# Optimization experiments

Hardware: AMD Instinct MI355X
Metric: run time of the kernel (lower is better)

Reference implementation:

```python
import jax, jax.numpy as jnp
import numpy as np

KH, KW = 3, 3
PAD = (1, 1, 1, 1)  # torch F.pad order: (W_left, W_right, H_top, H_bottom)
STRIDE = 1
B, CIN, COUT, H, W = 4, 32, 32, 128, 128


def setup_inputs() -> dict:
    key = jax.random.key(0)
    k1, k2, k3, k4 = jax.random.split(key, 4)
    f = jax.random.normal(k1, (B, CIN, H, W), jnp.float32)
    # orientation field components (cos/sin of a random angle field)
    theta = jax.random.uniform(k2, (B, CIN, H, W), jnp.float32, 0.0, 2.0 * np.pi)
    r0 = jnp.cos(theta)
    r1 = jnp.sin(theta)
    # learned conv weight (nn.Conv2d default uniform init, no bias)
    fan_in = CIN * KH * KW
    bound = 1.0 / np.sqrt(fan_in)
    w = jax.random.uniform(k3, (COUT, CIN, KH, KW), jnp.float32, -bound, bound)
    # frozen wr: (randn * pi * 100) / a with a = 100  ->  randn * pi
    wr = jax.random.normal(k4, (COUT, CIN, KH, KW), jnp.float32) * np.pi
    return {"f": f, "r0": r0, "r1": r1, "w": w, "wr": wr}


def _rot90(w):
    # torch: w.permute(0,1,2,4,3).flip([4]) on the (kh,kw) dims
    return jnp.flip(jnp.swapaxes(w, -1, -2), -1)


def _conv_single(f, r0, r1, w, wr):
    # f, r0, r1: (B, Cin, Hp, Wp);  w, wr: (Cout, Cin, KH, KW)
    Hp, Wp = f.shape[2], f.shape[3]
    he = Hp - PAD[0] - PAD[1]
    we = Wp - PAD[2] - PAD[3]
    s = STRIDE
    out = None
    for i in range(KH):
        for j in range(KW):
            fw = f[:, :, i:i + he:s, j:j + we:s]    # (B, Cin, h, w)
            r0w = r0[:, :, i:i + he:s, j:j + we:s]
            r1w = r1[:, :, i:i + he:s, j:j + we:s]
            c = jnp.cos(wr[:, :, i, j])[None, :, :, None, None]   # (1, Cout, Cin, 1, 1)
            sn = jnp.sin(wr[:, :, i, j])[None, :, :, None, None]
            # lambda_theta: relu of orientation-projected field, (B, Cout, Cin, h, w)
            lam = jax.nn.relu(c * r0w[:, None] + sn * r1w[:, None])
            term = jnp.einsum('bchw,oc,bochw->bohw', fw, w[:, :, i, j], lam)
            out = term if out is None else out + term
    return out  # (B, Cout, h, w)


def _forward(f, r0, r1, w, wr):
    pl, pr, pt, pb = PAD
    pad = ((0, 0), (0, 0), (pt, pb), (pl, pr))
    fp = jnp.pad(f, pad)
    r0p = jnp.pad(r0, pad)
    r1p = jnp.pad(r1, pad)
    orient = jnp.arange(4, dtype=f.dtype) * jnp.asarray(np.pi / 2, f.dtype)
    outs = []
    wk = w
    for o in range(4):
        if o > 0:
            wk = _rot90(wk)
        outs.append(_conv_single(fp, r0p, r1p, wk, wr + orient[o]))
    stacked = jnp.stack(outs, axis=2)              # (B, Cout, 4, h, w)
    idx = jnp.argmax(stacked, axis=2)              # (B, Cout, h, w)
    out = jnp.take_along_axis(stacked, idx[:, :, None], axis=2)[:, :, 0]
    out_r = orient[idx]                            # winning orientation angle
    return out, jnp.cos(out_r), jnp.sin(out_r)


def reference(f, r0, r1, w, wr):
    return _forward(f, r0, r1, w, wr)
```

## Files before the change

### kernel.cpp

```cpp
#include <hip/hip_runtime.h>


typedef float v2f __attribute__((ext_vector_type(2)));

#define B_    4
#define CIN_  32
#define COUT_ 32
#define H_    128
#define W_    128
#define HW_   (H_ * W_)
#define OUTSZ_ (B_ * COUT_ * H_ * W_)

__global__ __launch_bounds__(256)
void build_wtab(const float* __restrict__ w, const float* __restrict__ wr,
                float* __restrict__ tab)
{
    int idx = blockIdx.x * 256 + threadIdx.x;
    if (idx >= CIN_ * 9 * COUT_) return;
    int oc  = idx & 31;
    int t2  = idx >> 5;
    int tap = t2 % 9;
    int cc  = t2 / 9;
    int i = tap / 3, j = tap - i * 3;
    int base = (oc * CIN_ + cc) * 9;
    float w0 = w[base + i * 3 + j];
    float w1 = w[base + (2 - j) * 3 + i];
    float w2 = w[base + (2 - i) * 3 + (2 - j)];
    float w3 = w[base + j * 3 + (2 - i)];
    float S, C;
    sincosf(wr[base + i * 3 + j], &S, &C);
    float* dst = tab + (size_t)idx * 8;
    dst[0] = C;  dst[1] = S;
    dst[2] = w0; dst[3] = w1;
    dst[4] = w2; dst[5] = w3;
    dst[6] = 0.0f; dst[7] = 0.0f;
}

#define NC_    8
#define NG_    (CIN_ / NC_)
#define ROWF_  68
#define CLSTR_ (3 * ROWF_)
#define USED_  (NC_ * CLSTR_)
#define PLANE_ 1636
#define BUF_   (3 * PLANE_)

__global__ __launch_bounds__(512, 4)
void orient_conv_kernel(const float* __restrict__ f,
                        const float* __restrict__ r0,
                        const float* __restrict__ r1,
                        const float* __restrict__ tab,
                        float* __restrict__ out)
{
    __shared__ float sm[2 * BUF_];

    const int tid   = threadIdx.x;
    const int oc    = tid & 31;
    const int pxg   = tid >> 5;
    const int p     = pxg << 1;
    const int bid   = blockIdx.x;
    const int b     = bid >> 8;
    const int rem   = bid & 255;
    const int h     = rem >> 1;
    const int wbase = (rem & 1) << 6;

    int      goff[4], sidx[4];
    unsigned msk[4];
#pragma unroll
    for (int k = 0; k < 4; ++k) {
        int s = tid + (k << 9);
        if (s < USED_) {
            int cl  = s / CLSTR_;
            int r2  = s - cl * CLSTR_;
            int row = r2 / ROWF_;
            int q2  = r2 - row * ROWF_;
            int col = (q2 >> 1) + ((q2 & 1) << 5);
            int gh = h + row - 1;
            int gw = wbase + col - 1;
            bool ok = ((unsigned)gh < (unsigned)H_) & ((unsigned)gw < (unsigned)W_);
            goff[k] = ok ? (cl * HW_ + gh * W_ + gw) : 0;
            msk[k]  = ok ? 0xFFFFFFFFu : 0u;
            sidx[k] = s;
        } else { goff[k] = 0; msk[k] = 0u; sidx[k] = USED_; }
    }
    const bool have3 = (tid + 1536) < USED_;
    const int chanBase = b * (CIN_ * HW_);

    v2f acc[2][4];
#pragma unroll
    for (int q = 0; q < 2; ++q)
#pragma unroll
        for (int o = 0; o < 4; ++o) acc[q][o] = (v2f)(0.0f);

    float tF[4], tA[4], tB[4];
    {
        const float* fb = f  + chanBase;
        const float* ab = r0 + chanBase;
        const float* bb = r1 + chanBase;
#pragma unroll
        for (int k = 0; k < 3; ++k) {
            tF[k] = fb[goff[k]]; tA[k] = ab[goff[k]]; tB[k] = bb[goff[k]];
        }
        if (have3) { tF[3] = fb[goff[3]]; tA[3] = ab[goff[3]]; tB[3] = bb[goff[3]]; }
    }
    {
        float* bw = sm;
#pragma unroll
        for (int k = 0; k < 3; ++k) {
            bw[             sidx[k]] = __uint_as_float(__float_as_uint(tF[k]) & msk[k]);
            bw[PLANE_     + sidx[k]] = __uint_as_float(__float_as_uint(tA[k]) & msk[k]);
            bw[2 * PLANE_ + sidx[k]] = __uint_as_float(__float_as_uint(tB[k]) & msk[k]);
        }
        if (have3) {
            bw[             sidx[3]] = __uint_as_float(__float_as_uint(tF[3]) & msk[3]);
            bw[PLANE_     + sidx[3]] = __uint_as_float(__float_as_uint(tA[3]) & msk[3]);
            bw[2 * PLANE_ + sidx[3]] = __uint_as_float(__float_as_uint(tB[3]) & msk[3]);
        }
    }
    __syncthreads();

#pragma unroll 1
    for (int g = 0; g < NG_; ++g) {
        if (g + 1 < NG_) {
            const int gb = chanBase + (g + 1) * (NC_ * HW_);
            const float* fb = f  + gb;
            const float* ab = r0 + gb;
            const float* bb = r1 + gb;
#pragma unroll
            for (int k = 0; k < 3; ++k) {
                tF[k] = fb[goff[k]]; tA[k] = ab[goff[k]]; tB[k] = bb[goff[k]];
            }
            if (have3) { tF[3] = fb[goff[3]]; tA[3] = ab[goff[3]]; tB[3] = bb[goff[3]]; }
        }

        const float* br = sm + (g & 1) * BUF_;
#pragma unroll 1
        for (int cl = 0; cl < NC_; ++cl) {
            const int cc = g * NC_ + cl;
            const float* wb0 = tab + (size_t)(((cc * 9 + 2) << 5) | oc) * 8;
            const float* wb1 = wb0 + 4 * 256;
#pragma unroll
            for (int i = 0; i < 3; ++i) {
                const int bi = cl * CLSTR_ + i * ROWF_ + (p << 1);
                float4 fA = *reinterpret_cast<const float4*>(&br[bi]);
                float4 fB = *reinterpret_cast<const float4*>(&br[bi + 4]);
                float4 aA = *reinterpret_cast<const float4*>(&br[PLANE_ + bi]);
                float4 aB = *reinterpret_cast<const float4*>(&br[PLANE_ + bi + 4]);
                float4 bA = *reinterpret_cast<const float4*>(&br[2 * PLANE_ + bi]);
                float4 bB = *reinterpret_cast<const float4*>(&br[2 * PLANE_ + bi + 4]);
                v2f fP[4]  = {{fA.x, fA.y}, {fA.z, fA.w}, {fB.x, fB.y}, {fB.z, fB.w}};
                v2f aP[4]  = {{aA.x, aA.y}, {aA.z, aA.w}, {aB.x, aB.y}, {aB.z, aB.w}};
                v2f bP[4]  = {{bA.x, bA.y}, {bA.z, bA.w}, {bB.x, bB.y}, {bB.z, bB.w}};
#pragma unroll
                for (int j = 0; j < 3; ++j) {
                    const int tap = i * 3 + j;
                    const float* wp = (tap < 5) ? (wb0 + (tap - 2) * 256)
                                                : (wb1 + (tap - 6) * 256);
                    float4 W4 = *reinterpret_cast<const float4*>(wp);
                    float2 W2 = *reinterpret_cast<const float2*>(wp + 4);
                    v2f C2  = {W4.x, W4.x};
                    v2f S2  = {W4.y, W4.y};
                    v2f w02 = {W4.z, W4.z};
                    v2f w12 = {W4.w, W4.w};
                    v2f w22 = {W2.x, W2.x};
                    v2f w32 = {W2.y, W2.y};
#pragma unroll
                    for (int q = 0; q < 2; ++q) {
                        v2f fv  = fP[q + j];
                        v2f r0v = aP[q + j];
                        v2f r1v = bP[q + j];
                        v2f m1 = S2 * r1v;
                        v2f u  = __builtin_elementwise_fma(C2, r0v, m1);
                        v2f m2 = S2 * r0v;
                        v2f vv = __builtin_elementwise_fma(C2, r1v, -m2);
                        v2f g0 = __builtin_elementwise_max(u,  (v2f)(0.0f));
                        v2f g1 = __builtin_elementwise_max(vv, (v2f)(0.0f));
                        v2f t0 = fv * g0;
                        v2f t1 = fv * g1;
                        v2f t2 = __builtin_elementwise_fma(fv, -u,  t0);
                        v2f t3 = __builtin_elementwise_fma(fv, -vv, t1);
                        acc[q][0] = __builtin_elementwise_fma(t0, w02, acc[q][0]);
                        acc[q][1] = __builtin_elementwise_fma(t1, w12, acc[q][1]);
                        acc[q][2] = __builtin_elementwise_fma(t2, w22, acc[q][2]);
                        acc[q][3] = __builtin_elementwise_fma(t3, w32, acc[q][3]);
                    }
                }
            }
        }

        if (g + 1 < NG_) {
            float* bw = sm + ((g + 1) & 1) * BUF_;
#pragma unroll
            for (int k = 0; k < 3; ++k) {
                bw[             sidx[k]] = __uint_as_float(__float_as_uint(tF[k]) & msk[k]);
                bw[PLANE_     + sidx[k]] = __uint_as_float(__float_as_uint(tA[k]) & msk[k]);
                bw[2 * PLANE_ + sidx[k]] = __uint_as_float(__float_as_uint(tB[k]) & msk[k]);
            }
            if (have3) {
                bw[             sidx[3]] = __uint_as_float(__float_as_uint(tF[3]) & msk[3]);
                bw[PLANE_     + sidx[3]] = __uint_as_float(__float_as_uint(tA[3]) & msk[3]);
                bw[2 * PLANE_ + sidx[3]] = __uint_as_float(__float_as_uint(tB[3]) & msk[3]);
            }
            __syncthreads();
        }
    }

    const float cosv[4] = {1.0f, -4.37113883e-08f, -1.0f, 1.19248806e-08f};
    const float sinv[4] = {0.0f, 1.0f, -8.74227766e-08f, -1.0f};
#pragma unroll
    for (int q = 0; q < 2; ++q) {
#pragma unroll
        for (int k = 0; k < 2; ++k) {
            int wcol = wbase + p + q + (k << 5);
            float a0 = acc[q][0][k], a1 = acc[q][1][k];
            float a2 = acc[q][2][k], a3 = acc[q][3][k];
            float best = a0; int bi = 0;
            if (a1 > best) { best = a1; bi = 1; }
            if (a2 > best) { best = a2; bi = 2; }
            if (a3 > best) { best = a3; bi = 3; }
            size_t o = ((size_t)(b * COUT_ + oc) * H_ + h) * W_ + wcol;
            out[o]              = best;
            out[o + OUTSZ_]     = cosv[bi];
            out[o + 2 * OUTSZ_] = sinv[bi];
        }
    }
}

extern "C" void kernel_launch(void* const* d_in, const int* in_sizes, int n_in,
                              void* d_out, int out_size, void* d_ws, size_t ws_size,
                              hipStream_t stream)
{
    const float* f  = (const float*)d_in[0];
    const float* r0 = (const float*)d_in[1];
    const float* r1 = (const float*)d_in[2];
    const float* w  = (const float*)d_in[3];
    const float* wr = (const float*)d_in[4];
    float* out = (float*)d_out;
    float* tab = (float*)d_ws;

    build_wtab<<<dim3(36), dim3(256), 0, stream>>>(w, wr, tab);
    orient_conv_kernel<<<dim3(B_ * H_ * 2), dim3(512), 0, stream>>>(
        f, r0, r1, tab, out);
}
```

Measured before the change: 288.9 us.

## Compute two output rows per block to reuse staged input rows

Each block now loads a 4-row halo per channel instead of 3 and produces two output rows, so each shared-memory row read feeds both output rows' taps. This cuts redundant global and LDS input traffic per output by about a third and halves the block count. In exchange it doubles the accumulator registers, drops the min-blocks launch bound hint, and enlarges shared memory per block, which may reduce occupancy and leave fewer blocks to fill the GPU.

Result: slower. 507.4 us (+75.6%).

```diff
diff --git a/kernel.cpp b/kernel.cpp
--- a/kernel.cpp
+++ b/kernel.cpp
@@ -39,12 +39,14 @@
 #define NC_    8
 #define NG_    (CIN_ / NC_)
 #define ROWF_  68
-#define CLSTR_ (3 * ROWF_)
+#define NROW_  4
+#define CLSTR_ (NROW_ * ROWF_)
 #define USED_  (NC_ * CLSTR_)
-#define PLANE_ 1636
+#define PLANE_ 2180
 #define BUF_   (3 * PLANE_)
-
-__global__ __launch_bounds__(512, 4)
+#define NRND_  5
+
+__global__ __launch_bounds__(512)
 void orient_conv_kernel(const float* __restrict__ f,
                         const float* __restrict__ r0,
                         const float* __restrict__ r1,
@@ -58,15 +60,15 @@
     const int pxg   = tid >> 5;
     const int p     = pxg << 1;
     const int bid   = blockIdx.x;
-    const int b     = bid >> 8;
-    const int rem   = bid & 255;
-    const int h     = rem >> 1;
+    const int b     = bid >> 7;
+    const int rem   = bid & 127;
+    const int h0    = (rem >> 1) << 1;
     const int wbase = (rem & 1) << 6;
 
-    int      goff[4], sidx[4];
-    unsigned msk[4];
-#pragma unroll
-    for (int k = 0; k < 4; ++k) {
+    int      goff[NRND_], sidx[NRND_];
+    unsigned msk[NRND_];
+#pragma unroll
+    for (int k = 0; k < NRND_; ++k) {
         int s = tid + (k << 9);
         if (s < USED_) {
             int cl  = s / CLSTR_;
@@ -74,7 +76,7 @@
             int row = r2 / ROWF_;
             int q2  = r2 - row * ROWF_;
             int col = (q2 >> 1) + ((q2 & 1) << 5);
-            int gh = h + row - 1;
+            int gh = h0 + row - 1;
             int gw = wbase + col - 1;
             bool ok = ((unsigned)gh < (unsigned)H_) & ((unsigned)gw < (unsigned)W_);
             goff[k] = ok ? (cl * HW_ + gh * W_ + gw) : 0;
@@ -82,38 +84,42 @@
             sidx[k] = s;
         } else { goff[k] = 0; msk[k] = 0u; sidx[k] = USED_; }
     }
-    const bool have3 = (tid + 1536) < USED_;
+    const bool have4 = (tid + 2048) < USED_;
     const int chanBase = b * (CIN_ * HW_);
 
-    v2f acc[2][4];
-#pragma unroll
-    for (int q = 0; q < 2; ++q)
-#pragma unroll
-        for (int o = 0; o < 4; ++o) acc[q][o] = (v2f)(0.0f);
-
-    float tF[4], tA[4], tB[4];
+    v2f acc[2][2][4];
+#pragma unroll
+    for (int rr = 0; rr < 2; ++rr)
+#pragma unroll
+        for (int q = 0; q < 2; ++q)
+#pragma unroll
+            for (int o = 0; o < 4; ++o) acc[rr][q][o] = (v2f)(0.0f);
+
+    float tF[NRND_], tA[NRND_], tB[NRND_];
     {
         const float* fb = f  + chanBase;
         const float* ab = r0 + chanBase;
         const float* bb = r1 + chanBase;
 #pragma unroll
-        for (int k = 0; k < 3; ++k) {
+        for (int k = 0; k < NRND_ - 1; ++k) {
             tF[k] = fb[goff[k]]; tA[k] = ab[goff[k]]; tB[k] = bb[goff[k]];
         }
-        if (have3) { tF[3] = fb[goff[3]]; tA[3] = ab[goff[3]]; tB[3] = bb[goff[3]]; }
+        if (have4) {
+            tF[4] = fb[goff[4]]; tA[4] = ab[goff[4]]; tB[4] = bb[goff[4]];
+        }
     }
     {
         float* bw = sm;
 #pragma unroll
-        for (int k = 0; k < 3; ++k) {
+        for (int k = 0; k < NRND_ - 1; ++k) {
             bw[             sidx[k]] = __uint_as_float(__float_as_uint(tF[k]) & msk[k]);
             bw[PLANE_     + sidx[k]] = __uint_as_float(__float_as_uint(tA[k]) & msk[k]);
             bw[2 * PLANE_ + sidx[k]] = __uint_as_float(__float_as_uint(tB[k]) & msk[k]);
         }
-        if (have3) {
-            bw[             sidx[3]] = __uint_as_float(__float_as_uint(tF[3]) & msk[3]);
-            bw[PLANE_     + sidx[3]] = __uint_as_float(__float_as_uint(tA[3]) & msk[3]);
-            bw[2 * PLANE_ + sidx[3]] = __uint_as_float(__float_as_uint(tB[3]) & msk[3]);
+        if (have4) {
+            bw[             sidx[4]] = __uint_as_float(__float_as_uint(tF[4]) & msk[4]);
+            bw[PLANE_     + sidx[4]] = __uint_as_float(__float_as_uint(tA[4]) & msk[4]);
+            bw[2 * PLANE_ + sidx[4]] = __uint_as_float(__float_as_uint(tB[4]) & msk[4]);
         }
     }
     __syncthreads();
@@ -126,10 +132,12 @@
             const float* ab = r0 + gb;
             const float* bb = r1 + gb;
 #pragma unroll
-            for (int k = 0; k < 3; ++k) {
+            for (int k = 0; k < NRND_ - 1; ++k) {
                 tF[k] = fb[goff[k]]; tA[k] = ab[goff[k]]; tB[k] = bb[goff[k]];
             }
-            if (have3) { tF[3] = fb[goff[3]]; tA[3] = ab[goff[3]]; tB[3] = bb[goff[3]]; }
+            if (have4) {
+                tF[4] = fb[goff[4]]; tA[4] = ab[goff[4]]; tB[4] = bb[goff[4]];
+            }
         }
 
         const float* br = sm + (g & 1) * BUF_;
@@ -139,8 +147,8 @@
             const float* wb0 = tab + (size_t)(((cc * 9 + 2) << 5) | oc) * 8;
             const float* wb1 = wb0 + 4 * 256;
 #pragma unroll
-            for (int i = 0; i < 3; ++i) {
-                const int bi = cl * CLSTR_ + i * ROWF_ + (p << 1);
+            for (int r = 0; r < NROW_; ++r) {
+                const int bi = cl * CLSTR_ + r * ROWF_ + (p << 1);
                 float4 fA = *reinterpret_cast<const float4*>(&br[bi]);
                 float4 fB = *reinterpret_cast<const float4*>(&br[bi + 4]);
                 float4 aA = *reinterpret_cast<const float4*>(&br[PLANE_ + bi]);
@@ -150,55 +158,60 @@
                 v2f fP[4]  = {{fA.x, fA.y}, {fA.z, fA.w}, {fB.x, fB.y}, {fB.z, fB.w}};
                 v2f aP[4]  = {{aA.x, aA.y}, {aA.z, aA.w}, {aB.x, aB.y}, {aB.z, aB.w}};
                 v2f bP[4]  = {{bA.x, bA.y}, {bA.z, bA.w}, {bB.x, bB.y}, {bB.z, bB.w}};
-#pragma unroll
-                for (int j = 0; j < 3; ++j) {
-                    const int tap = i * 3 + j;
-                    const float* wp = (tap < 5) ? (wb0 + (tap - 2) * 256)
-                                                : (wb1 + (tap - 6) * 256);
-                    float4 W4 = *reinterpret_cast<const float4*>(wp);
-                    float2 W2 = *reinterpret_cast<const float2*>(wp + 4);
-                    v2f C2  = {W4.x, W4.x};
-                    v2f S2  = {W4.y, W4.y};
-                    v2f w02 = {W4.z, W4.z};
-                    v2f w12 = {W4.w, W4.w};
-                    v2f w22 = {W2.x, W2.x};
-                    v2f w32 = {W2.y, W2.y};
-#pragma unroll
-                    for (int q = 0; q < 2; ++q) {
-                        v2f fv  = fP[q + j];
-                        v2f r0v = aP[q + j];
-                        v2f r1v = bP[q + j];
-                        v2f m1 = S2 * r1v;
-                        v2f u  = __builtin_elementwise_fma(C2, r0v, m1);
-                        v2f m2 = S2 * r0v;
-                        v2f vv = __builtin_elementwise_fma(C2, r1v, -m2);
-                        v2f g0 = __builtin_elementwise_max(u,  (v2f)(0.0f));
-                        v2f g1 = __builtin_elementwise_max(vv, (v2f)(0.0f));
-                        v2f t0 = fv * g0;
-                        v2f t1 = fv * g1;
-                        v2f t2 = __builtin_elementwise_fma(fv, -u,  t0);
-                        v2f t3 = __builtin_elementwise_fma(fv, -vv, t1);
-                        acc[q][0] = __builtin_elementwise_fma(t0, w02, acc[q][0]);
-                        acc[q][1] = __builtin_elementwise_fma(t1, w12, acc[q][1]);
-                        acc[q][2] = __builtin_elementwise_fma(t2, w22, acc[q][2]);
-                        acc[q][3] = __builtin_elementwise_fma(t3, w32, acc[q][3]);
+
+                auto apply = [&](int ti, int rr) {
+#pragma unroll
+                    for (int j = 0; j < 3; ++j) {
+                        const int tap = ti * 3 + j;
+                        const float* wp = (tap < 5) ? (wb0 + (tap - 2) * 256)
+                                                    : (wb1 + (tap - 6) * 256);
+                        float4 W4 = *reinterpret_cast<const float4*>(wp);
+                        float2 W2 = *reinterpret_cast<const float2*>(wp + 4);
+                        v2f C2  = {W4.x, W4.x};
+                        v2f S2  = {W4.y, W4.y};
+                        v2f w02 = {W4.z, W4.z};
+                        v2f w12 = {W4.w, W4.w};
+                        v2f w22 = {W2.x, W2.x};
+                        v2f w32 = {W2.y, W2.y};
+#pragma unroll
+                        for (int q = 0; q < 2; ++q) {
+                            v2f fv  = fP[q + j];
+                            v2f r0v = aP[q + j];
+                            v2f r1v = bP[q + j];
+                            v2f m1 = S2 * r1v;
+                            v2f u  = __builtin_elementwise_fma(C2, r0v, m1);
+                            v2f m2 = S2 * r0v;
+                            v2f vv = __builtin_elementwise_fma(C2, r1v, -m2);
+                            v2f g0 = __builtin_elementwise_max(u,  (v2f)(0.0f));
+                            v2f g1 = __builtin_elementwise_max(vv, (v2f)(0.0f));
+                            v2f t0 = fv * g0;
+                            v2f t1 = fv * g1;
+                            v2f t2 = __builtin_elementwise_fma(fv, -u,  t0);
+                            v2f t3 = __builtin_elementwise_fma(fv, -vv, t1);
+                            acc[rr][q][0] = __builtin_elementwise_fma(t0, w02, acc[rr][q][0]);
+                            acc[rr][q][1] = __builtin_elementwise_fma(t1, w12, acc[rr][q][1]);
+                            acc[rr][q][2] = __builtin_elementwise_fma(t2, w22, acc[rr][q][2]);
+                            acc[rr][q][3] = __builtin_elementwise_fma(t3, w32, acc[rr][q][3]);
+                        }
                     }
-                }
+                };
+                if (r < 3) apply(r, 0);
+                if (r > 0) apply(r - 1, 1);
             }
         }
 
         if (g + 1 < NG_) {
             float* bw = sm + ((g + 1) & 1) * BUF_;
 #pragma unroll
-            for (int k = 0; k < 3; ++k) {
+            for (int k = 0; k < NRND_ - 1; ++k) {
                 bw[             sidx[k]] = __uint_as_float(__float_as_uint(tF[k]) & msk[k]);
                 bw[PLANE_     + sidx[k]] = __uint_as_float(__float_as_uint(tA[k]) & msk[k]);
                 bw[2 * PLANE_ + sidx[k]] = __uint_as_float(__float_as_uint(tB[k]) & msk[k]);
             }
-            if (have3) {
-                bw[             sidx[3]] = __uint_as_float(__float_as_uint(tF[3]) & msk[3]);
-                bw[PLANE_     + sidx[3]] = __uint_as_float(__float_as_uint(tA[3]) & msk[3]);
-                bw[2 * PLANE_ + sidx[3]] = __uint_as_float(__float_as_uint(tB[3]) & msk[3]);
+            if (have4) {
+                bw[             sidx[4]] = __uint_as_float(__float_as_uint(tF[4]) & msk[4]);
+                bw[PLANE_     + sidx[4]] = __uint_as_float(__float_as_uint(tA[4]) & msk[4]);
+                bw[2 * PLANE_ + sidx[4]] = __uint_as_float(__float_as_uint(tB[4]) & msk[4]);
             }
             __syncthreads();
         }
@@ -207,20 +220,23 @@
     const float cosv[4] = {1.0f, -4.37113883e-08f, -1.0f, 1.19248806e-08f};
     const float sinv[4] = {0.0f, 1.0f, -8.74227766e-08f, -1.0f};
 #pragma unroll
-    for (int q = 0; q < 2; ++q) {
-#pragma unroll
-        for (int k = 0; k < 2; ++k) {
-            int wcol = wbase + p + q + (k << 5);
-            float a0 = acc[q][0][k], a1 = acc[q][1][k];
-            float a2 = acc[q][2][k], a3 = acc[q][3][k];
-            float best = a0; int bi = 0;
-            if (a1 > best) { best = a1; bi = 1; }
-            if (a2 > best) { best = a2; bi = 2; }
-            if (a3 > best) { best = a3; bi = 3; }
-            size_t o = ((size_t)(b * COUT_ + oc) * H_ + h) * W_ + wcol;
-            out[o]              = best;
-            out[o + OUTSZ_]     = cosv[bi];
-            out[o + 2 * OUTSZ_] = sinv[bi];
+    for (int rr = 0; rr < 2; ++rr) {
+#pragma unroll
+        for (int q = 0; q < 2; ++q) {
+#pragma unroll
+            for (int k = 0; k < 2; ++k) {
+                int wcol = wbase + p + q + (k << 5);
+                float a0 = acc[rr][q][0][k], a1 = acc[rr][q][1][k];
+                float a2 = acc[rr][q][2][k], a3 = acc[rr][q][3][k];
+                float best = a0; int bi = 0;
+                if (a1 > best) { best = a1; bi = 1; }
+                if (a2 > best) { best = a2; bi = 2; }
+                if (a3 > best) { best = a3; bi = 3; }
+                size_t o = ((size_t)(b * COUT_ + oc) * H_ + (h0 + rr)) * W_ + wcol;
+                out[o]              = best;
+                out[o + OUTSZ_]     = cosv[bi];
+                out[o + 2 * OUTSZ_] = sinv[bi];
+            }
         }
     }
 }
@@ -238,6 +254,6 @@
     float* tab = (float*)d_ws;
 
     build_wtab<<<dim3(36), dim3(256), 0, stream>>>(w, wr, tab);
-    orient_conv_kernel<<<dim3(B_ * H_ * 2), dim3(512), 0, stream>>>(
+    orient_conv_kernel<<<dim3(B_ * H_), dim3(512), 0, stream>>>(
         f, r0, r1, tab, out);
 }
```
